# Kernel optimization log

Measured on AMD Instinct MI355X. Metric: run time of the kernel, lower is better.

The kernel has to match this reference:

```python
import jax, jax.numpy as jnp
import numpy as np
import math

BS, SEQ, DIM, H, LK = 4, 4096, 768, 12, 256
HD = DIM // H  # 64
WIN = SEQ // LK  # 16, AdaptiveAvgPool1d reduces to uniform windows since SEQ % LK == 0


def setup_inputs() -> dict:
    key = jax.random.key(0)
    ks = jax.random.split(key, 12)
    s = 1.0 / math.sqrt(DIM)
    return {
        "query": jax.random.normal(ks[0], (BS, SEQ, DIM), jnp.float32),
        "key": jax.random.normal(ks[1], (BS, SEQ, DIM), jnp.float32),
        "value": jax.random.normal(ks[2], (BS, SEQ, DIM), jnp.float32),
        "mask": jax.random.normal(ks[3], (BS, SEQ), jnp.float32),  # mask<0 -> padded
        "Wq": jax.random.normal(ks[4], (DIM, DIM), jnp.float32) * s,
        "bq": jnp.zeros((DIM,), jnp.float32),
        "Wk": jax.random.normal(ks[5], (DIM, DIM), jnp.float32) * s,
        "bk": jnp.zeros((DIM,), jnp.float32),
        "Wv": jax.random.normal(ks[6], (DIM, DIM), jnp.float32) * s,
        "bv": jnp.zeros((DIM,), jnp.float32),
        "Wo": jax.random.normal(ks[7], (DIM, DIM), jnp.float32) * s,
        "bo": jnp.zeros((DIM,), jnp.float32),
    }


def reference(query, key, value, mask, Wq, bq, Wk, bk, Wv, bv, Wo, bo):
    bs, q_len, _ = query.shape
    # projections (nn.Linear: x @ W.T + b)
    Q = query @ Wq.T + bq
    K = key @ Wk.T + bk
    V = value @ Wv.T + bv
    # mask-fill padded K/V rows with 0 (mask dim==2 path: bool_mask = mask < 0)
    keep = (mask >= 0)[:, :, None]  # [bs, seq, 1]
    K = jnp.where(keep, K, 0.0)
    V = jnp.where(keep, V, 0.0)
    # adaptive avg pool over sequence -> linformer_k=256 (uniform windows of 16)
    Kc = K.reshape(bs, LK, WIN, DIM).mean(axis=2)  # [bs, 256, dim]
    Vc = V.reshape(bs, LK, WIN, DIM).mean(axis=2)
    # split heads
    Qh = Q.reshape(bs, q_len, H, HD) / math.sqrt(HD)  # scale fused
    Kh = Kc.reshape(bs, LK, H, HD)
    Vh = Vc.reshape(bs, LK, H, HD)
    # low-rank attention: [bs, h, q_len, 256]
    scores = jnp.einsum("bqhd,bkhd->bhqk", Qh, Kh)
    weights = jax.nn.softmax(scores, axis=-1)
    context = jnp.einsum("bhqk,bkhd->bqhd", weights, Vh).reshape(bs, q_len, DIM)
    return context @ Wo.T + bo
```

## Files before the change

### kernel.cpp

```cpp
#include <hip/hip_runtime.h>

#define BS_   4
#define SEQ_  4096
#define DIM_  768
#define NH_   12
#define HD_   64
#define LK_   256

typedef __attribute__((ext_vector_type(8))) short          bf8;
typedef __attribute__((ext_vector_type(8))) unsigned short us8;
typedef __attribute__((ext_vector_type(4))) unsigned short us4;
typedef __attribute__((ext_vector_type(4))) float          f32x4;

typedef unsigned int u32g __attribute__((address_space(1)));
typedef unsigned int u32l __attribute__((address_space(3)));

#define LOG2E 1.44269504088896340736f

__device__ __forceinline__ unsigned short f2bf(float f) {
  unsigned u = __builtin_bit_cast(unsigned, f);
  u += 0x7fffu + ((u >> 16) & 1u);
  return (unsigned short)(u >> 16);
}

__device__ __forceinline__ us8 cvt8(const float* __restrict__ p) {
  const float4 a = *(const float4*)p;
  const float4 b = *(const float4*)(p + 4);
  us8 r;
  r[0] = f2bf(a.x); r[1] = f2bf(a.y); r[2] = f2bf(a.z); r[3] = f2bf(a.w);
  r[4] = f2bf(b.x); r[5] = f2bf(b.y); r[6] = f2bf(b.z); r[7] = f2bf(b.w);
  return r;
}

__device__ __forceinline__ f32x4 max4(f32x4 a, f32x4 b) {
  f32x4 r;
  r[0] = fmaxf(a[0], b[0]); r[1] = fmaxf(a[1], b[1]);
  r[2] = fmaxf(a[2], b[2]); r[3] = fmaxf(a[3], b[3]);
  return r;
}

__global__ __launch_bounds__(256) void cvtbf_kernel(
    const float* __restrict__ query,
    const float* __restrict__ Wq, const float* __restrict__ Wk,
    const float* __restrict__ Wv, const float* __restrict__ Wo,
    unsigned short* __restrict__ Qbf, unsigned short* __restrict__ Wbf)
{
  const int i = blockIdx.x * 256 + threadIdx.x;
  const int QN8 = (BS_ * SEQ_ * DIM_) / 8;
  const int WN8 = (DIM_ * DIM_) / 8;
  if (i < QN8) { *(us8*)(Qbf + (size_t)i * 8) = cvt8(query + (size_t)i * 8); return; }
  int j = i - QN8;
  const float* src; unsigned short* dst;
  if      (j <     WN8) { src = Wq; dst = Wbf;                   }
  else if (j < 2 * WN8) { src = Wk; dst = Wbf + DIM_*DIM_;     j -=     WN8; }
  else if (j < 3 * WN8) { src = Wv; dst = Wbf + 2*DIM_*DIM_;   j -= 2 * WN8; }
  else if (j < 4 * WN8) { src = Wo; dst = Wbf + 3*DIM_*DIM_;   j -= 3 * WN8; }
  else return;
  *(us8*)(dst + (size_t)j * 8) = cvt8(src + (size_t)j * 8);
}

__global__ __launch_bounds__(384) void pool_kernel(
    const float* __restrict__ key, const float* __restrict__ value,
    const float* __restrict__ mask,
    unsigned short* __restrict__ pk, unsigned short* __restrict__ pv,
    float* __restrict__ frac)
{
  const int blk = blockIdx.x;
  const int b = blk >> 8;
  const int l = blk & 255;
  const int tid = threadIdx.x;
  __shared__ float keep[16];
  if (tid < 16) keep[tid] = (mask[b * SEQ_ + l * 16 + tid] >= 0.f) ? 1.f : 0.f;
  __syncthreads();
  const int isV = tid >= 192;
  const int c = isV ? tid - 192 : tid;
  const float* src = isV ? value : key;
  float4 acc = make_float4(0.f, 0.f, 0.f, 0.f);
  #pragma unroll 1
  for (int w = 0; w < 16; ++w) {
    if (keep[w] != 0.f) {
      const float4 v = *(const float4*)(src + (size_t)(b * SEQ_ + l * 16 + w) * DIM_ + c * 4);
      acc.x += v.x; acc.y += v.y; acc.z += v.z; acc.w += v.w;
    }
  }
  const float s = 1.f / 16.f;
  unsigned short* dst = isV ? pv : pk;
  us4 o4;
  o4[0] = f2bf(acc.x * s); o4[1] = f2bf(acc.y * s);
  o4[2] = f2bf(acc.z * s); o4[3] = f2bf(acc.w * s);
  *(us4*)(dst + (size_t)(b * LK_ + l) * DIM_ + c * 4) = o4;
  if (tid == 0) {
    float cnt = 0.f;
    for (int w = 0; w < 16; ++w) cnt += keep[w];
    frac[b * LK_ + l] = cnt * s;
  }
}

template<int MODE, int SWZ>
__global__ __launch_bounds__(256) void gemm_bt(
    const void* __restrict__ Aptr_, const void* __restrict__ Bptr_,
    const float* __restrict__ bias, const float* __restrict__ bias2,
    const float* __restrict__ frac,
    void* __restrict__ Cout, float scale)
{
  constexpr int K  = DIM_;
  constexpr int BK = 64;
  constexpr int NT = K / BK;
  __shared__ __align__(16) unsigned short lA[128 * BK];
  __shared__ __align__(16) unsigned short lB[128 * BK];
  const int tid  = threadIdx.x;
  const int lane = tid & 63;
  const int wave = tid >> 6;

  int bx, by;
  if (SWZ) {
    const int r = (blockIdx.x & 7) * 96 + (blockIdx.x >> 3);
    bx = r / 6; by = r % 6;
  } else {
    bx = blockIdx.x; by = blockIdx.y;
  }
  const int brow = bx * 128;
  const int bcol = by * 128;

  const unsigned short* A  = (const unsigned short*)Aptr_;
  const unsigned short* Bw = (const unsigned short*)Bptr_;
  const float* bb = bias;
  int isV = 0;
  if (MODE == 34) {
    isV = blockIdx.z;
    A  += (size_t)isV * (BS_ * LK_ * DIM_);
    Bw += (size_t)isV * (DIM_ * DIM_);
    if (isV) bb = bias2;
  }

  const int wr = (wave >> 1) * 64;
  const int wc = (wave & 1) * 64;
  const int fr = lane & 15;
  const int hi = lane >> 4;
  const int rx = fr & 7;

  f32x4 acc[4][4];
  #pragma unroll
  for (int i = 0; i < 4; ++i)
    #pragma unroll
    for (int j = 0; j < 4; ++j) acc[i][j] = (f32x4){0.f, 0.f, 0.f, 0.f};

  const int srow = tid >> 3;
  const int schk = ((tid & 7) ^ (srow & 7)) * 8;

  for (int t = 0; t < NT; ++t) {
    const int k0 = t * BK;
    __syncthreads();
    #pragma unroll
    for (int s = 0; s < 4; ++s) {
      __builtin_amdgcn_global_load_lds(
          (const u32g*)(A + (size_t)(brow + srow + s * 32) * K + k0 + schk),
          (u32l*)&lA[s * 2048 + tid * 8], 16, 0, 0);
      __builtin_amdgcn_global_load_lds(
          (const u32g*)(Bw + (size_t)(bcol + srow + s * 32) * K + k0 + schk),
          (u32l*)&lB[s * 2048 + tid * 8], 16, 0, 0);
    }
    __syncthreads();
    #pragma unroll
    for (int ks = 0; ks < 2; ++ks) {
      bf8 af[4], bfv[4];
      const int c = ks * 4 + hi;
      const int pc = (c ^ rx) * 8;
      #pragma unroll
      for (int mi = 0; mi < 4; ++mi)
        af[mi] = *(const bf8*)&lA[(wr + mi * 16 + fr) * BK + pc];
      #pragma unroll
      for (int ni = 0; ni < 4; ++ni)
        bfv[ni] = *(const bf8*)&lB[(wc + ni * 16 + fr) * BK + pc];
      #pragma unroll
      for (int mi = 0; mi < 4; ++mi)
        #pragma unroll
        for (int ni = 0; ni < 4; ++ni)
          acc[mi][ni] = __builtin_amdgcn_mfma_f32_16x16x32_bf16(af[mi], bfv[ni], acc[mi][ni], 0, 0, 0);
    }
  }

  const int er = (lane >> 4) * 4;
  #pragma unroll
  for (int mi = 0; mi < 4; ++mi) {
    #pragma unroll
    for (int ni = 0; ni < 4; ++ni) {
      #pragma unroll
      for (int j = 0; j < 4; ++j) {
        const int r = brow + wr + mi * 16 + er + j;
        const int c = bcol + wc + ni * 16 + fr;
        float v = acc[mi][ni][j];
        if (MODE == 0) {
          v = (v + bias[c]) * scale;
          ((unsigned short*)Cout)[(size_t)r * DIM_ + c] = f2bf(v);
        } else if (MODE == 2) {
          ((float*)Cout)[(size_t)r * DIM_ + c] = v + bias[c];
        } else {
          v += frac[r] * bb[c];
          const int bb_ = r >> 8, key = r & 255;
          const int hh = c >> 6, dd = c & 63;
          const int bh = bb_ * NH_ + hh;
          size_t idx;
          if (isV) {
            idx = (size_t)bh * 16384 +
                ((key >> 5) * 4 + (dd >> 4)) * 512 + ((key >> 3) & 3) * 128 +
                (dd & 15) * 8 + (key & 7) + 786432;
          } else {
            const int tt = key >> 5, g = (key >> 3) & 3, sub = (key >> 2) & 1, jj = key & 3;
            const int frk = g * 4 + jj;
            idx = (size_t)bh * 16384 +
                (((tt * 2 + sub) * 2) + (dd >> 5)) * 512 + ((dd >> 3) & 3) * 128 +
                frk * 8 + (dd & 7);
          }
          ((unsigned short*)Cout)[idx] = f2bf(v);
        }
      }
    }
  }
}

__global__ __launch_bounds__(1024, 4) void attn_fused(
    const unsigned short* __restrict__ Qh,
    const unsigned short* __restrict__ Kf,
    const unsigned short* __restrict__ Vf,
    unsigned short* __restrict__ ctx)
{
  __shared__ __align__(16) unsigned short Ks[16384];
  __shared__ __align__(16) unsigned short Vs[16384];
  const int tid  = threadIdx.x;
  const int lane = tid & 63;
  const int wave = tid >> 6;
  const int bh = blockIdx.y;
  const int b = bh / NH_, h = bh % NH_;
  const int fr = lane & 15;
  const int hi = lane >> 4;
  const int qrow = blockIdx.x * 256 + wave * 16;

  {
    const unsigned short* kg = Kf + (size_t)bh * 16384 + tid * 8;
    const unsigned short* vg = Vf + (size_t)bh * 16384 + tid * 8;
    __builtin_amdgcn_global_load_lds((const u32g*)kg,          (u32l*)&Ks[tid * 8],        16, 0, 0);
    __builtin_amdgcn_global_load_lds((const u32g*)(kg + 8192), (u32l*)&Ks[8192 + tid * 8], 16, 0, 0);
    __builtin_amdgcn_global_load_lds((const u32g*)vg,          (u32l*)&Vs[tid * 8],        16, 0, 0);
    __builtin_amdgcn_global_load_lds((const u32g*)(vg + 8192), (u32l*)&Vs[8192 + tid * 8], 16, 0, 0);
  }

  const unsigned short* qp = Qh + (size_t)(b * SEQ_ + qrow + fr) * DIM_ + h * HD_ + hi * 8;
  const bf8 q0 = *(const bf8*)qp;
  const bf8 q1 = *(const bf8*)(qp + 32);

  __syncthreads();

  f32x4 scA[8], scB[8];
  __builtin_amdgcn_s_setprio(1);
  #pragma unroll
  for (int s = 0; s < 8; ++s) {
    const bf8 ka0 = *(const bf8*)&Ks[(s * 4 + 0) * 512 + lane * 8];
    const bf8 ka1 = *(const bf8*)&Ks[(s * 4 + 1) * 512 + lane * 8];
    const bf8 kb0 = *(const bf8*)&Ks[(s * 4 + 2) * 512 + lane * 8];
    const bf8 kb1 = *(const bf8*)&Ks[(s * 4 + 3) * 512 + lane * 8];
    f32x4 x = (f32x4){0.f, 0.f, 0.f, 0.f};
    x = __builtin_amdgcn_mfma_f32_16x16x32_bf16(ka0, q0, x, 0, 0, 0);
    x = __builtin_amdgcn_mfma_f32_16x16x32_bf16(ka1, q1, x, 0, 0, 0);
    scA[s] = x;
    f32x4 y = (f32x4){0.f, 0.f, 0.f, 0.f};
    y = __builtin_amdgcn_mfma_f32_16x16x32_bf16(kb0, q0, y, 0, 0, 0);
    y = __builtin_amdgcn_mfma_f32_16x16x32_bf16(kb1, q1, y, 0, 0, 0);
    scB[s] = y;
  }
  __builtin_amdgcn_s_setprio(0);

  f32x4 tm[8];
  #pragma unroll
  for (int s = 0; s < 8; ++s) tm[s] = max4(scA[s], scB[s]);
  tm[0] = max4(tm[0], tm[4]); tm[1] = max4(tm[1], tm[5]);
  tm[2] = max4(tm[2], tm[6]); tm[3] = max4(tm[3], tm[7]);
  tm[0] = max4(tm[0], tm[2]); tm[1] = max4(tm[1], tm[3]);
  tm[0] = max4(tm[0], tm[1]);
  float m = fmaxf(fmaxf(tm[0][0], tm[0][1]), fmaxf(tm[0][2], tm[0][3]));
  m = fmaxf(m, __shfl_xor(m, 16));
  m = fmaxf(m, __shfl_xor(m, 32));

  f32x4 uA = (f32x4){0.f, 0.f, 0.f, 0.f};
  f32x4 uB = (f32x4){0.f, 0.f, 0.f, 0.f};
  #pragma unroll
  for (int s = 0; s < 8; ++s) {
    #pragma unroll
    for (int j = 0; j < 4; ++j) {
      scA[s][j] = exp2f(scA[s][j] - m);
      scB[s][j] = exp2f(scB[s][j] - m);
    }
    uA += scA[s];
    uB += scB[s];
  }
  const f32x4 uv = uA + uB;
  float sum = (uv[0] + uv[1]) + (uv[2] + uv[3]);
  sum += __shfl_xor(sum, 16);
  sum += __shfl_xor(sum, 32);
  const float inv = 1.f / sum;

  bf8 pa[8];
  #pragma unroll
  for (int s = 0; s < 8; ++s) {
    bf8 p;
    #pragma unroll
    for (int j = 0; j < 4; ++j) {
      p[j]     = (short)f2bf(scA[s][j] * inv);
      p[4 + j] = (short)f2bf(scB[s][j] * inv);
    }
    pa[s] = p;
  }

  f32x4 acc[4];
  #pragma unroll
  for (int ct = 0; ct < 4; ++ct) acc[ct] = (f32x4){0.f, 0.f, 0.f, 0.f};
  __builtin_amdgcn_s_setprio(1);
  #pragma unroll
  for (int s = 0; s < 8; ++s) {
    #pragma unroll
    for (int ct = 0; ct < 4; ++ct) {
      const bf8 vf = *(const bf8*)&Vs[(s * 4 + ct) * 512 + lane * 8];
      acc[ct] = __builtin_amdgcn_mfma_f32_16x16x32_bf16(pa[s], vf, acc[ct], 0, 0, 0);
    }
  }
  __builtin_amdgcn_s_setprio(0);

  #pragma unroll
  for (int ct = 0; ct < 4; ++ct)
    #pragma unroll
    for (int j = 0; j < 4; ++j)
      ctx[(size_t)(b * SEQ_ + qrow + hi * 4 + j) * DIM_ + h * HD_ + ct * 16 + fr] =
          f2bf(acc[ct][j]);
}

extern "C" void kernel_launch(void* const* d_in, const int* in_sizes, int n_in,
                              void* d_out, int out_size, void* d_ws, size_t ws_size,
                              hipStream_t stream) {
  const float* query = (const float*)d_in[0];
  const float* key   = (const float*)d_in[1];
  const float* value = (const float*)d_in[2];
  const float* mask  = (const float*)d_in[3];
  const float* Wq    = (const float*)d_in[4];
  const float* bq    = (const float*)d_in[5];
  const float* Wk    = (const float*)d_in[6];
  const float* bk    = (const float*)d_in[7];
  const float* Wv    = (const float*)d_in[8];
  const float* bv    = (const float*)d_in[9];
  const float* Wo    = (const float*)d_in[10];
  const float* bo    = (const float*)d_in[11];
  float* out = (float*)d_out;

  char* ws = (char*)d_ws;
  unsigned short* Qh  = (unsigned short*)ws;
  unsigned short* ctx = (unsigned short*)(ws + 25165824);
  unsigned short* pK  = (unsigned short*)(ws + 50331648);
  unsigned short* pV  = (unsigned short*)(ws + 51904512);
  unsigned short* Kf  = (unsigned short*)(ws + 53477376);
  unsigned short* Vf  = (unsigned short*)(ws + 55050240);
  float*          frac = (float*)(ws + 56623104);
  unsigned short* Wbf = (unsigned short*)(ws + 56627200);
  unsigned short* Qbf = ctx;

  const float qscale = 0.125f * LOG2E;

  pool_kernel<<<dim3(1024), dim3(384), 0, stream>>>(key, value, mask, pK, pV, frac);
  cvtbf_kernel<<<dim3(7296), dim3(256), 0, stream>>>(query, Wq, Wk, Wv, Wo, Qbf, Wbf);
  gemm_bt<0, 1><<<dim3(768), dim3(256), 0, stream>>>(
      Qbf, Wbf, bq, nullptr, nullptr, Qh, qscale);
  gemm_bt<34, 0><<<dim3(8, 6, 2), dim3(256), 0, stream>>>(
      pK, Wbf + DIM_*DIM_, bk, bv, frac, Kf, 1.f);
  attn_fused<<<dim3(16, 48), dim3(1024), 0, stream>>>(Qh, Kf, Vf, ctx);
  gemm_bt<2, 1><<<dim3(768), dim3(256), 0, stream>>>(
      ctx, Wbf + 3*DIM_*DIM_, bo, nullptr, nullptr, out, 1.f);
}
```

Measured before the change: 140.5 us.

## Fuse prep and QKV GEMM launches, read V directly from global in attention

Pooling and bf16 conversion are merged into one prep kernel, and the Q projection and pooled K/V projections run in a single grid, cutting launch count and letting the small K/V GEMM overlap the large Q GEMM. The attention kernel stops staging V in LDS and loads V fragments from global/L2 during the PV MFMA loop. This halves LDS use per block but adds global-load latency inside the inner loop.

```diff
diff --git a/kernel.cpp b/kernel.cpp
--- a/kernel.cpp
+++ b/kernel.cpp
@@ -39,15 +39,50 @@
   return r;
 }
 
-__global__ __launch_bounds__(256) void cvtbf_kernel(
-    const float* __restrict__ query,
+__global__ __launch_bounds__(384) void prep_kernel(
+    const float* __restrict__ key, const float* __restrict__ value,
+    const float* __restrict__ mask, const float* __restrict__ query,
     const float* __restrict__ Wq, const float* __restrict__ Wk,
     const float* __restrict__ Wv, const float* __restrict__ Wo,
+    unsigned short* __restrict__ pk, unsigned short* __restrict__ pv,
+    float* __restrict__ frac,
     unsigned short* __restrict__ Qbf, unsigned short* __restrict__ Wbf)
 {
-  const int i = blockIdx.x * 256 + threadIdx.x;
+  const int bid = blockIdx.x;
+  const int tid = threadIdx.x;
+  if (bid < 1024) {
+    const int b = bid >> 8;
+    const int l = bid & 255;
+    __shared__ float keep[16];
+    if (tid < 16) keep[tid] = (mask[b * SEQ_ + l * 16 + tid] >= 0.f) ? 1.f : 0.f;
+    __syncthreads();
+    const int isV = tid >= 192;
+    const int c = isV ? tid - 192 : tid;
+    const float* src = isV ? value : key;
+    float4 acc = make_float4(0.f, 0.f, 0.f, 0.f);
+    #pragma unroll 1
+    for (int w = 0; w < 16; ++w) {
+      if (keep[w] != 0.f) {
+        const float4 v = *(const float4*)(src + (size_t)(b * SEQ_ + l * 16 + w) * DIM_ + c * 4);
+        acc.x += v.x; acc.y += v.y; acc.z += v.z; acc.w += v.w;
+      }
+    }
+    const float s = 1.f / 16.f;
+    unsigned short* dst = isV ? pv : pk;
+    us4 o4;
+    o4[0] = f2bf(acc.x * s); o4[1] = f2bf(acc.y * s);
+    o4[2] = f2bf(acc.z * s); o4[3] = f2bf(acc.w * s);
+    *(us4*)(dst + (size_t)(b * LK_ + l) * DIM_ + c * 4) = o4;
+    if (tid == 0) {
+      float cnt = 0.f;
+      for (int w = 0; w < 16; ++w) cnt += keep[w];
+      frac[b * LK_ + l] = cnt * s;
+    }
+    return;
+  }
   const int QN8 = (BS_ * SEQ_ * DIM_) / 8;
   const int WN8 = (DIM_ * DIM_) / 8;
+  const int i = (bid - 1024) * 384 + tid;
   if (i < QN8) { *(us8*)(Qbf + (size_t)i * 8) = cvt8(query + (size_t)i * 8); return; }
   int j = i - QN8;
   const float* src; unsigned short* dst;
@@ -59,49 +94,13 @@
   *(us8*)(dst + (size_t)j * 8) = cvt8(src + (size_t)j * 8);
 }
 
-__global__ __launch_bounds__(384) void pool_kernel(
-    const float* __restrict__ key, const float* __restrict__ value,
-    const float* __restrict__ mask,
-    unsigned short* __restrict__ pk, unsigned short* __restrict__ pv,
-    float* __restrict__ frac)
-{
-  const int blk = blockIdx.x;
-  const int b = blk >> 8;
-  const int l = blk & 255;
-  const int tid = threadIdx.x;
-  __shared__ float keep[16];
-  if (tid < 16) keep[tid] = (mask[b * SEQ_ + l * 16 + tid] >= 0.f) ? 1.f : 0.f;
-  __syncthreads();
-  const int isV = tid >= 192;
-  const int c = isV ? tid - 192 : tid;
-  const float* src = isV ? value : key;
-  float4 acc = make_float4(0.f, 0.f, 0.f, 0.f);
-  #pragma unroll 1
-  for (int w = 0; w < 16; ++w) {
-    if (keep[w] != 0.f) {
-      const float4 v = *(const float4*)(src + (size_t)(b * SEQ_ + l * 16 + w) * DIM_ + c * 4);
-      acc.x += v.x; acc.y += v.y; acc.z += v.z; acc.w += v.w;
-    }
-  }
-  const float s = 1.f / 16.f;
-  unsigned short* dst = isV ? pv : pk;
-  us4 o4;
-  o4[0] = f2bf(acc.x * s); o4[1] = f2bf(acc.y * s);
-  o4[2] = f2bf(acc.z * s); o4[3] = f2bf(acc.w * s);
-  *(us4*)(dst + (size_t)(b * LK_ + l) * DIM_ + c * 4) = o4;
-  if (tid == 0) {
-    float cnt = 0.f;
-    for (int w = 0; w < 16; ++w) cnt += keep[w];
-    frac[b * LK_ + l] = cnt * s;
-  }
-}
-
-template<int MODE, int SWZ>
-__global__ __launch_bounds__(256) void gemm_bt(
-    const void* __restrict__ Aptr_, const void* __restrict__ Bptr_,
-    const float* __restrict__ bias, const float* __restrict__ bias2,
-    const float* __restrict__ frac,
-    void* __restrict__ Cout, float scale)
+__global__ __launch_bounds__(256) void gemm_qkv(
+    const unsigned short* __restrict__ Qbf, const unsigned short* __restrict__ pKV,
+    const unsigned short* __restrict__ Wbf,
+    const float* __restrict__ bq, const float* __restrict__ bk,
+    const float* __restrict__ bv, const float* __restrict__ frac,
+    unsigned short* __restrict__ Qh, unsigned short* __restrict__ KVf,
+    float qscale)
 {
   constexpr int K  = DIM_;
   constexpr int BK = 64;
@@ -111,27 +110,27 @@
   const int tid  = threadIdx.x;
   const int lane = tid & 63;
   const int wave = tid >> 6;
-
-  int bx, by;
-  if (SWZ) {
-    const int r = (blockIdx.x & 7) * 96 + (blockIdx.x >> 3);
+  const int bid  = blockIdx.x;
+  const int isQ  = bid < 768;
+
+  int bx, by, isV = 0;
+  const unsigned short* A;
+  const unsigned short* Bw;
+  if (isQ) {
+    const int r = (bid & 7) * 96 + (bid >> 3);
     bx = r / 6; by = r % 6;
+    A  = Qbf;
+    Bw = Wbf;
   } else {
-    bx = blockIdx.x; by = blockIdx.y;
+    int kid = bid - 768;
+    isV = kid >= 48;
+    kid -= isV * 48;
+    bx = kid / 6; by = kid % 6;
+    A  = pKV + (size_t)isV * (BS_ * LK_ * DIM_);
+    Bw = Wbf + (size_t)(1 + isV) * (DIM_ * DIM_);
   }
   const int brow = bx * 128;
   const int bcol = by * 128;
-
-  const unsigned short* A  = (const unsigned short*)Aptr_;
-  const unsigned short* Bw = (const unsigned short*)Bptr_;
-  const float* bb = bias;
-  int isV = 0;
-  if (MODE == 34) {
-    isV = blockIdx.z;
-    A  += (size_t)isV * (BS_ * LK_ * DIM_);
-    Bw += (size_t)isV * (DIM_ * DIM_);
-    if (isV) bb = bias2;
-  }
 
   const int wr = (wave >> 1) * 64;
   const int wc = (wave & 1) * 64;
@@ -190,13 +189,11 @@
         const int r = brow + wr + mi * 16 + er + j;
         const int c = bcol + wc + ni * 16 + fr;
         float v = acc[mi][ni][j];
-        if (MODE == 0) {
-          v = (v + bias[c]) * scale;
-          ((unsigned short*)Cout)[(size_t)r * DIM_ + c] = f2bf(v);
-        } else if (MODE == 2) {
-          ((float*)Cout)[(size_t)r * DIM_ + c] = v + bias[c];
+        if (isQ) {
+          v = (v + bq[c]) * qscale;
+          Qh[(size_t)r * DIM_ + c] = f2bf(v);
         } else {
-          v += frac[r] * bb[c];
+          v += frac[r] * (isV ? bv[c] : bk[c]);
           const int bb_ = r >> 8, key = r & 255;
           const int hh = c >> 6, dd = c & 63;
           const int bh = bb_ * NH_ + hh;
@@ -212,11 +209,86 @@
                 (((tt * 2 + sub) * 2) + (dd >> 5)) * 512 + ((dd >> 3) & 3) * 128 +
                 frk * 8 + (dd & 7);
           }
-          ((unsigned short*)Cout)[idx] = f2bf(v);
+          KVf[idx] = f2bf(v);
         }
       }
     }
   }
+}
+
+__global__ __launch_bounds__(256) void gemm_out(
+    const unsigned short* __restrict__ A, const unsigned short* __restrict__ Bw,
+    const float* __restrict__ bias, float* __restrict__ Cout)
+{
+  constexpr int K  = DIM_;
+  constexpr int BK = 64;
+  constexpr int NT = K / BK;
+  __shared__ __align__(16) unsigned short lA[128 * BK];
+  __shared__ __align__(16) unsigned short lB[128 * BK];
+  const int tid  = threadIdx.x;
+  const int lane = tid & 63;
+  const int wave = tid >> 6;
+  const int r0 = (blockIdx.x & 7) * 96 + (blockIdx.x >> 3);
+  const int brow = (r0 / 6) * 128;
+  const int bcol = (r0 % 6) * 128;
+  const int wr = (wave >> 1) * 64;
+  const int wc = (wave & 1) * 64;
+  const int fr = lane & 15;
+  const int hi = lane >> 4;
+  const int rx = fr & 7;
+
+  f32x4 acc[4][4];
+  #pragma unroll
+  for (int i = 0; i < 4; ++i)
+    #pragma unroll
+    for (int j = 0; j < 4; ++j) acc[i][j] = (f32x4){0.f, 0.f, 0.f, 0.f};
+
+  const int srow = tid >> 3;
+  const int schk = ((tid & 7) ^ (srow & 7)) * 8;
+
+  for (int t = 0; t < NT; ++t) {
+    const int k0 = t * BK;
+    __syncthreads();
+    #pragma unroll
+    for (int s = 0; s < 4; ++s) {
+      __builtin_amdgcn_global_load_lds(
+          (const u32g*)(A + (size_t)(brow + srow + s * 32) * K + k0 + schk),
+          (u32l*)&lA[s * 2048 + tid * 8], 16, 0, 0);
+      __builtin_amdgcn_global_load_lds(
+          (const u32g*)(Bw + (size_t)(bcol + srow + s * 32) * K + k0 + schk),
+          (u32l*)&lB[s * 2048 + tid * 8], 16, 0, 0);
+    }
+    __syncthreads();
+    #pragma unroll
+    for (int ks = 0; ks < 2; ++ks) {
+      bf8 af[4], bfv[4];
+      const int c = ks * 4 + hi;
+      const int pc = (c ^ rx) * 8;
+      #pragma unroll
+      for (int mi = 0; mi < 4; ++mi)
+        af[mi] = *(const bf8*)&lA[(wr + mi * 16 + fr) * BK + pc];
+      #pragma unroll
+      for (int ni = 0; ni < 4; ++ni)
+        bfv[ni] = *(const bf8*)&lB[(wc + ni * 16 + fr) * BK + pc];
+      #pragma unroll
+      for (int mi = 0; mi < 4; ++mi)
+        #pragma unroll
+        for (int ni = 0; ni < 4; ++ni)
+          acc[mi][ni] = __builtin_amdgcn_mfma_f32_16x16x32_bf16(af[mi], bfv[ni], acc[mi][ni], 0, 0, 0);
+    }
+  }
+
+  const int er = (lane >> 4) * 4;
+  #pragma unroll
+  for (int mi = 0; mi < 4; ++mi)
+    #pragma unroll
+    for (int ni = 0; ni < 4; ++ni)
+      #pragma unroll
+      for (int j = 0; j < 4; ++j) {
+        const int r = brow + wr + mi * 16 + er + j;
+        const int c = bcol + wc + ni * 16 + fr;
+        Cout[(size_t)r * DIM_ + c] = acc[mi][ni][j] + bias[c];
+      }
 }
 
 __global__ __launch_bounds__(1024, 4) void attn_fused(
@@ -226,7 +298,6 @@
     unsigned short* __restrict__ ctx)
 {
   __shared__ __align__(16) unsigned short Ks[16384];
-  __shared__ __align__(16) unsigned short Vs[16384];
   const int tid  = threadIdx.x;
   const int lane = tid & 63;
   const int wave = tid >> 6;
@@ -238,11 +309,8 @@
 
   {
     const unsigned short* kg = Kf + (size_t)bh * 16384 + tid * 8;
-    const unsigned short* vg = Vf + (size_t)bh * 16384 + tid * 8;
     __builtin_amdgcn_global_load_lds((const u32g*)kg,          (u32l*)&Ks[tid * 8],        16, 0, 0);
     __builtin_amdgcn_global_load_lds((const u32g*)(kg + 8192), (u32l*)&Ks[8192 + tid * 8], 16, 0, 0);
-    __builtin_amdgcn_global_load_lds((const u32g*)vg,          (u32l*)&Vs[tid * 8],        16, 0, 0);
-    __builtin_amdgcn_global_load_lds((const u32g*)(vg + 8192), (u32l*)&Vs[8192 + tid * 8], 16, 0, 0);
   }
 
   const unsigned short* qp = Qh + (size_t)(b * SEQ_ + qrow + fr) * DIM_ + h * HD_ + hi * 8;
@@ -311,6 +379,7 @@
     pa[s] = p;
   }
 
+  const unsigned short* vb = Vf + (size_t)bh * 16384 + lane * 8;
   f32x4 acc[4];
   #pragma unroll
   for (int ct = 0; ct < 4; ++ct) acc[ct] = (f32x4){0.f, 0.f, 0.f, 0.f};
@@ -319,7 +388,7 @@
   for (int s = 0; s < 8; ++s) {
     #pragma unroll
     for (int ct = 0; ct < 4; ++ct) {
-      const bf8 vf = *(const bf8*)&Vs[(s * 4 + ct) * 512 + lane * 8];
+      const bf8 vf = *(const bf8*)(vb + (s * 4 + ct) * 512);
       acc[ct] = __builtin_amdgcn_mfma_f32_16x16x32_bf16(pa[s], vf, acc[ct], 0, 0, 0);
     }
   }
@@ -363,13 +432,10 @@
 
   const float qscale = 0.125f * LOG2E;
 
-  pool_kernel<<<dim3(1024), dim3(384), 0, stream>>>(key, value, mask, pK, pV, frac);
-  cvtbf_kernel<<<dim3(7296), dim3(256), 0, stream>>>(query, Wq, Wk, Wv, Wo, Qbf, Wbf);
-  gemm_bt<0, 1><<<dim3(768), dim3(256), 0, stream>>>(
-      Qbf, Wbf, bq, nullptr, nullptr, Qh, qscale);
-  gemm_bt<34, 0><<<dim3(8, 6, 2), dim3(256), 0, stream>>>(
-      pK, Wbf + DIM_*DIM_, bk, bv, frac, Kf, 1.f);
+  prep_kernel<<<dim3(5888), dim3(384), 0, stream>>>(
+      key, value, mask, query, Wq, Wk, Wv, Wo, pK, pV, frac, Qbf, Wbf);
+  gemm_qkv<<<dim3(864), dim3(256), 0, stream>>>(
+      Qbf, pK, Wbf, bq, bk, bv, frac, Qh, Kf, qscale);
   attn_fused<<<dim3(16, 48), dim3(1024), 0, stream>>>(Qh, Kf, Vf, ctx);
-  gemm_bt<2, 1><<<dim3(768), dim3(256), 0, stream>>>(
-      ctx, Wbf + 3*DIM_*DIM_, bo, nullptr, nullptr, out, 1.f);
-}
+  gemm_out<<<dim3(768), dim3(256), 0, stream>>>(ctx, Wbf + 3*DIM_*DIM_, bo, out);
+}
```

After: 138.3 us. Within noise of the previous version (-1.6%).

## Merge pool and bf16 conversion kernels; read V fragments directly from global

Applied to the files above, without the earlier changes.

Folds the pooling kernel and the fp32-to-bf16 conversion kernel into a single launch that dispatches on block index, removing one kernel launch and its tail. In the attention kernel, V is no longer staged in LDS; each wave loads its V fragments straight from global memory (L2-cached), halving LDS use to raise occupancy. The trade-off is repeated global loads of V by all 16 waves per block, plus a mixed-shape grid in the prep kernel.

```diff
diff --git a/kernel.cpp b/kernel.cpp
--- a/kernel.cpp
+++ b/kernel.cpp
@@ -39,15 +39,50 @@
   return r;
 }
 
-__global__ __launch_bounds__(256) void cvtbf_kernel(
-    const float* __restrict__ query,
+__global__ __launch_bounds__(384) void prep_kernel(
+    const float* __restrict__ key, const float* __restrict__ value,
+    const float* __restrict__ mask, const float* __restrict__ query,
     const float* __restrict__ Wq, const float* __restrict__ Wk,
     const float* __restrict__ Wv, const float* __restrict__ Wo,
+    unsigned short* __restrict__ pk, unsigned short* __restrict__ pv,
+    float* __restrict__ frac,
     unsigned short* __restrict__ Qbf, unsigned short* __restrict__ Wbf)
 {
-  const int i = blockIdx.x * 256 + threadIdx.x;
+  const int bid = blockIdx.x;
+  const int tid = threadIdx.x;
+  if (bid < 1024) {
+    const int b = bid >> 8;
+    const int l = bid & 255;
+    __shared__ float keep[16];
+    if (tid < 16) keep[tid] = (mask[b * SEQ_ + l * 16 + tid] >= 0.f) ? 1.f : 0.f;
+    __syncthreads();
+    const int isV = tid >= 192;
+    const int c = isV ? tid - 192 : tid;
+    const float* src = isV ? value : key;
+    float4 acc = make_float4(0.f, 0.f, 0.f, 0.f);
+    #pragma unroll 1
+    for (int w = 0; w < 16; ++w) {
+      if (keep[w] != 0.f) {
+        const float4 v = *(const float4*)(src + (size_t)(b * SEQ_ + l * 16 + w) * DIM_ + c * 4);
+        acc.x += v.x; acc.y += v.y; acc.z += v.z; acc.w += v.w;
+      }
+    }
+    const float s = 1.f / 16.f;
+    unsigned short* dst = isV ? pv : pk;
+    us4 o4;
+    o4[0] = f2bf(acc.x * s); o4[1] = f2bf(acc.y * s);
+    o4[2] = f2bf(acc.z * s); o4[3] = f2bf(acc.w * s);
+    *(us4*)(dst + (size_t)(b * LK_ + l) * DIM_ + c * 4) = o4;
+    if (tid == 0) {
+      float cnt = 0.f;
+      for (int w = 0; w < 16; ++w) cnt += keep[w];
+      frac[b * LK_ + l] = cnt * s;
+    }
+    return;
+  }
   const int QN8 = (BS_ * SEQ_ * DIM_) / 8;
   const int WN8 = (DIM_ * DIM_) / 8;
+  const int i = (bid - 1024) * 384 + tid;
   if (i < QN8) { *(us8*)(Qbf + (size_t)i * 8) = cvt8(query + (size_t)i * 8); return; }
   int j = i - QN8;
   const float* src; unsigned short* dst;
@@ -57,43 +92,6 @@
   else if (j < 4 * WN8) { src = Wo; dst = Wbf + 3*DIM_*DIM_;   j -= 3 * WN8; }
   else return;
   *(us8*)(dst + (size_t)j * 8) = cvt8(src + (size_t)j * 8);
-}
-
-__global__ __launch_bounds__(384) void pool_kernel(
-    const float* __restrict__ key, const float* __restrict__ value,
-    const float* __restrict__ mask,
-    unsigned short* __restrict__ pk, unsigned short* __restrict__ pv,
-    float* __restrict__ frac)
-{
-  const int blk = blockIdx.x;
-  const int b = blk >> 8;
-  const int l = blk & 255;
-  const int tid = threadIdx.x;
-  __shared__ float keep[16];
-  if (tid < 16) keep[tid] = (mask[b * SEQ_ + l * 16 + tid] >= 0.f) ? 1.f : 0.f;
-  __syncthreads();
-  const int isV = tid >= 192;
-  const int c = isV ? tid - 192 : tid;
-  const float* src = isV ? value : key;
-  float4 acc = make_float4(0.f, 0.f, 0.f, 0.f);
-  #pragma unroll 1
-  for (int w = 0; w < 16; ++w) {
-    if (keep[w] != 0.f) {
-      const float4 v = *(const float4*)(src + (size_t)(b * SEQ_ + l * 16 + w) * DIM_ + c * 4);
-      acc.x += v.x; acc.y += v.y; acc.z += v.z; acc.w += v.w;
-    }
-  }
-  const float s = 1.f / 16.f;
-  unsigned short* dst = isV ? pv : pk;
-  us4 o4;
-  o4[0] = f2bf(acc.x * s); o4[1] = f2bf(acc.y * s);
-  o4[2] = f2bf(acc.z * s); o4[3] = f2bf(acc.w * s);
-  *(us4*)(dst + (size_t)(b * LK_ + l) * DIM_ + c * 4) = o4;
-  if (tid == 0) {
-    float cnt = 0.f;
-    for (int w = 0; w < 16; ++w) cnt += keep[w];
-    frac[b * LK_ + l] = cnt * s;
-  }
 }
 
 template<int MODE, int SWZ>
@@ -226,7 +224,6 @@
     unsigned short* __restrict__ ctx)
 {
   __shared__ __align__(16) unsigned short Ks[16384];
-  __shared__ __align__(16) unsigned short Vs[16384];
   const int tid  = threadIdx.x;
   const int lane = tid & 63;
   const int wave = tid >> 6;
@@ -238,11 +235,8 @@
 
   {
     const unsigned short* kg = Kf + (size_t)bh * 16384 + tid * 8;
-    const unsigned short* vg = Vf + (size_t)bh * 16384 + tid * 8;
     __builtin_amdgcn_global_load_lds((const u32g*)kg,          (u32l*)&Ks[tid * 8],        16, 0, 0);
     __builtin_amdgcn_global_load_lds((const u32g*)(kg + 8192), (u32l*)&Ks[8192 + tid * 8], 16, 0, 0);
-    __builtin_amdgcn_global_load_lds((const u32g*)vg,          (u32l*)&Vs[tid * 8],        16, 0, 0);
-    __builtin_amdgcn_global_load_lds((const u32g*)(vg + 8192), (u32l*)&Vs[8192 + tid * 8], 16, 0, 0);
   }
 
   const unsigned short* qp = Qh + (size_t)(b * SEQ_ + qrow + fr) * DIM_ + h * HD_ + hi * 8;
@@ -311,6 +305,7 @@
     pa[s] = p;
   }
 
+  const unsigned short* vb = Vf + (size_t)bh * 16384 + lane * 8;
   f32x4 acc[4];
   #pragma unroll
   for (int ct = 0; ct < 4; ++ct) acc[ct] = (f32x4){0.f, 0.f, 0.f, 0.f};
@@ -319,7 +314,7 @@
   for (int s = 0; s < 8; ++s) {
     #pragma unroll
     for (int ct = 0; ct < 4; ++ct) {
-      const bf8 vf = *(const bf8*)&Vs[(s * 4 + ct) * 512 + lane * 8];
+      const bf8 vf = *(const bf8*)(vb + (s * 4 + ct) * 512);
       acc[ct] = __builtin_amdgcn_mfma_f32_16x16x32_bf16(pa[s], vf, acc[ct], 0, 0, 0);
     }
   }
@@ -363,8 +358,8 @@
 
   const float qscale = 0.125f * LOG2E;
 
-  pool_kernel<<<dim3(1024), dim3(384), 0, stream>>>(key, value, mask, pK, pV, frac);
-  cvtbf_kernel<<<dim3(7296), dim3(256), 0, stream>>>(query, Wq, Wk, Wv, Wo, Qbf, Wbf);
+  prep_kernel<<<dim3(5888), dim3(384), 0, stream>>>(
+      key, value, mask, query, Wq, Wk, Wv, Wo, pK, pV, frac, Qbf, Wbf);
   gemm_bt<0, 1><<<dim3(768), dim3(256), 0, stream>>>(
       Qbf, Wbf, bq, nullptr, nullptr, Qh, qscale);
   gemm_bt<34, 0><<<dim3(8, 6, 2), dim3(256), 0, stream>>>(
```

After: 137.2 us. 2.3% less time.
